# Optimization experiments

Measured on AMD Instinct MI355X. Metric: run time of the kernel, lower is better.

The kernel has to match this reference:

```python
import jax, jax.numpy as jnp
from jax import lax
import numpy as np

EPS = 1e-10


def setup_inputs() -> dict:
    key = jax.random.key(0)
    B, C, F, T = 32, 2, 257, 2000
    x = jax.random.uniform(key, (B, C, F, T), dtype=jnp.float32)  # magnitude-like, positive
    return {"input": x, "sample_length": 192}


def reference(input, sample_length):
    # Faithful jax version of BaseModel.forgetting_norm.
    # input: [B, C, F, T]
    B, C, F, T = input.shape
    x = input.reshape(B, C * F, T)
    dt = x.dtype
    # per-frame mean over channel*freq: [B, T]
    frame_mean = jnp.mean(x, axis=1)
    alpha = jnp.asarray((sample_length - 1) / (sample_length + 1), dtype=dt)
    idx = jnp.arange(T, dtype=dt)
    # torch code: alp = min((i-1)/(i+1), alpha); for i >= sample_length this equals alpha
    alp = jnp.minimum((idx - 1.0) / (idx + 1.0), alpha)  # [T]

    def step(mu, inp):
        a, m = inp  # scalars broadcast over batch: a [], m [B]
        mu = a * mu + (1.0 - a) * m
        return mu, mu

    mu0 = jnp.zeros((B,), dtype=dt)
    _, mus = lax.scan(step, mu0, (alp, frame_mean.T))  # mus: [T, B]
    mu = mus.T  # [B, T]
    out = x / (mu[:, None, :] + EPS)
    return out.reshape(B, C, F, T)
```

## Files before the change

### kernel.cpp

```cpp
#include <hip/hip_runtime.h>

#define EPS 1e-10f

constexpr int B  = 32;
constexpr int CF = 514;
constexpr int T  = 2000;
constexpr int T4 = T / 4;

__global__ __launch_bounds__(512) void k_frame_mean(const float* __restrict__ x,
                                                    float* __restrict__ fm) {
    __shared__ float lds[8][64];
    const int t  = blockIdx.x * 64 + threadIdx.x;
    const int b  = blockIdx.y;
    const int ty = threadIdx.y;

    float s = 0.0f;
    if (t < T) {
        const float* p = x + ((size_t)b * CF + ty) * T + t;
        #pragma unroll 4
        for (int cf = ty; cf < CF; cf += 8) {
            s += *p;
            p += 8 * (size_t)T;
        }
    }
    lds[ty][threadIdx.x] = s;
    __syncthreads();
    if (ty == 0 && t < T) {
        float tot = lds[0][threadIdx.x];
        #pragma unroll
        for (int k = 1; k < 8; ++k) tot += lds[k][threadIdx.x];
        fm[(size_t)b * T + t] = tot / (float)CF;
    }
}

__global__ __launch_bounds__(256) void k_scan_par(const float* __restrict__ fm,
                                                  const int* __restrict__ d_sl,
                                                  float* __restrict__ mu_out) {
    const int wave = threadIdx.x >> 6;
    const int lane = threadIdx.x & 63;
    const int b    = blockIdx.x * 4 + wave;
    if (b >= B) return;

    const int sl = d_sl[0];
    const float alpha = (float)((double)(sl - 1) / (double)(sl + 1));

    const float* __restrict__ m = fm + (size_t)b * T;
    float* __restrict__ o = mu_out + (size_t)b * T;

    const int t0 = lane * 32;

    float v[32];
    if (t0 + 32 <= T) {
        #pragma unroll
        for (int j = 0; j < 8; ++j)
            *(float4*)(v + 4 * j) = *(const float4*)(m + t0 + 4 * j);
    } else {
        #pragma unroll
        for (int j = 0; j < 32; ++j)
            v[j] = (t0 + j < T) ? m[t0 + j] : 0.0f;
    }

    float A = 1.0f, Bv = 0.0f;
    #pragma unroll
    for (int i = 0; i < 32; ++i) {
        const int t = t0 + i;
        const float ft = (float)t;
        const float a  = (t < T) ? fminf((ft - 1.0f) / (ft + 1.0f), alpha) : 1.0f;
        const float vv = (t < T) ? v[i] : 0.0f;
        Bv = a * Bv + (1.0f - a) * vv;
        A  = a * A;
    }

    float pA = A, pB = Bv;
    #pragma unroll
    for (int d = 1; d < 64; d <<= 1) {
        const float uA = __shfl_up(pA, d);
        const float uB = __shfl_up(pB, d);
        if (lane >= d) {
            pB = pA * uB + pB;
            pA = pA * uA;
        }
    }

    const float eB = __shfl_up(pB, 1);
    float mu = (lane == 0) ? 0.0f : eB;

    #pragma unroll
    for (int i = 0; i < 32; ++i) {
        const int t = t0 + i;
        if (t < T) {
            const float ft = (float)t;
            const float a  = fminf((ft - 1.0f) / (ft + 1.0f), alpha);
            mu = a * mu + (1.0f - a) * v[i];
            o[t] = mu;
        }
    }
}

__global__ __launch_bounds__(256) void k_norm(const float4* __restrict__ x,
                                              const float* __restrict__ mu,
                                              float4* __restrict__ out) {
    const int t4  = blockIdx.x * 256 + threadIdx.x;
    if (t4 >= T4) return;
    const int row = blockIdx.y;
    const int b   = row / CF;

    const size_t idx = (size_t)row * T4 + t4;
    const float4 v  = x[idx];
    const float4 m4 = *(const float4*)(mu + (size_t)b * T + (size_t)t4 * 4);

    float4 r;
    r.x = v.x / (m4.x + EPS);
    r.y = v.y / (m4.y + EPS);
    r.z = v.z / (m4.z + EPS);
    r.w = v.w / (m4.w + EPS);
    out[idx] = r;
}

extern "C" void kernel_launch(void* const* d_in, const int* in_sizes, int n_in,
                              void* d_out, int out_size, void* d_ws, size_t ws_size,
                              hipStream_t stream) {
    const float* x    = (const float*)d_in[0];
    const int*   d_sl = (const int*)d_in[1];
    float*       out  = (float*)d_out;

    float* fm = (float*)d_ws;
    float* mu = fm + (size_t)B * T;

    {
        dim3 grid((T + 63) / 64, B);
        dim3 block(64, 8);
        k_frame_mean<<<grid, block, 0, stream>>>(x, fm);
    }
    {
        k_scan_par<<<8, 256, 0, stream>>>(fm, d_sl, mu);
    }
    {
        dim3 grid((T4 + 255) / 256, B * CF);
        dim3 block(256);
        k_norm<<<grid, block, 0, stream>>>((const float4*)x, mu, (float4*)out);
    }
}
```

Measured before the change: 258.4 us.

## Fuse scan into normalization kernel with per-block redundant scan

```diff
diff --git a/kernel.cpp b/kernel.cpp
--- a/kernel.cpp
+++ b/kernel.cpp
@@ -5,7 +5,6 @@
 constexpr int B  = 32;
 constexpr int CF = 514;
 constexpr int T  = 2000;
-constexpr int T4 = T / 4;
 
 __global__ __launch_bounds__(512) void k_frame_mean(const float* __restrict__ x,
                                                     float* __restrict__ fm) {
@@ -33,88 +32,85 @@
     }
 }
 
-__global__ __launch_bounds__(256) void k_scan_par(const float* __restrict__ fm,
-                                                  const int* __restrict__ d_sl,
-                                                  float* __restrict__ mu_out) {
-    const int wave = threadIdx.x >> 6;
-    const int lane = threadIdx.x & 63;
-    const int b    = blockIdx.x * 4 + wave;
-    if (b >= B) return;
+__global__ __launch_bounds__(256) void k_scan_norm(const float* __restrict__ x,
+                                                   const float* __restrict__ fm,
+                                                   const int* __restrict__ d_sl,
+                                                   float* __restrict__ out) {
+    __shared__ float mu_win[64];
+    const int tx  = threadIdx.x & 63;
+    const int ty  = threadIdx.x >> 6;
+    const int bid = blockIdx.x;
+    const int b   = bid >> 5;
+    const int t0  = (bid & 31) * 64;
 
-    const int sl = d_sl[0];
-    const float alpha = (float)((double)(sl - 1) / (double)(sl + 1));
+    if (ty == 0) {
+        const int lane = tx;
+        const int sl   = d_sl[0];
+        const float alpha = (float)((double)(sl - 1) / (double)(sl + 1));
+        const float* __restrict__ m = fm + (size_t)b * T;
+        const int ts = lane * 32;
 
-    const float* __restrict__ m = fm + (size_t)b * T;
-    float* __restrict__ o = mu_out + (size_t)b * T;
+        float v[32];
+        if (ts + 32 <= T) {
+            #pragma unroll
+            for (int j = 0; j < 8; ++j)
+                *(float4*)(v + 4 * j) = *(const float4*)(m + ts + 4 * j);
+        } else {
+            #pragma unroll
+            for (int j = 0; j < 32; ++j)
+                v[j] = (ts + j < T) ? m[ts + j] : 0.0f;
+        }
 
-    const int t0 = lane * 32;
+        float A = 1.0f, Bv = 0.0f;
+        #pragma unroll
+        for (int i = 0; i < 32; ++i) {
+            const int tt = ts + i;
+            const float ft = (float)tt;
+            const float a  = (tt < T) ? fminf((ft - 1.0f) / (ft + 1.0f), alpha) : 1.0f;
+            const float vv = (tt < T) ? v[i] : 0.0f;
+            Bv = a * Bv + (1.0f - a) * vv;
+            A  = a * A;
+        }
 
-    float v[32];
-    if (t0 + 32 <= T) {
+        float pA = A, pB = Bv;
         #pragma unroll
-        for (int j = 0; j < 8; ++j)
-            *(float4*)(v + 4 * j) = *(const float4*)(m + t0 + 4 * j);
-    } else {
+        for (int d = 1; d < 64; d <<= 1) {
+            const float uA = __shfl_up(pA, d);
+            const float uB = __shfl_up(pB, d);
+            if (lane >= d) {
+                pB = pA * uB + pB;
+                pA = pA * uA;
+            }
+        }
+
+        const float eB = __shfl_up(pB, 1);
+        float muv = (lane == 0) ? 0.0f : eB;
+
         #pragma unroll
-        for (int j = 0; j < 32; ++j)
-            v[j] = (t0 + j < T) ? m[t0 + j] : 0.0f;
-    }
-
-    float A = 1.0f, Bv = 0.0f;
-    #pragma unroll
-    for (int i = 0; i < 32; ++i) {
-        const int t = t0 + i;
-        const float ft = (float)t;
-        const float a  = (t < T) ? fminf((ft - 1.0f) / (ft + 1.0f), alpha) : 1.0f;
-        const float vv = (t < T) ? v[i] : 0.0f;
-        Bv = a * Bv + (1.0f - a) * vv;
-        A  = a * A;
-    }
-
-    float pA = A, pB = Bv;
-    #pragma unroll
-    for (int d = 1; d < 64; d <<= 1) {
-        const float uA = __shfl_up(pA, d);
-        const float uB = __shfl_up(pB, d);
-        if (lane >= d) {
-            pB = pA * uB + pB;
-            pA = pA * uA;
+        for (int i = 0; i < 32; ++i) {
+            const int tt = ts + i;
+            if (tt < T) {
+                const float ft = (float)tt;
+                const float a  = fminf((ft - 1.0f) / (ft + 1.0f), alpha);
+                muv = a * muv + (1.0f - a) * v[i];
+                if (tt >= t0 && tt < t0 + 64) mu_win[tt - t0] = muv;
+            }
         }
     }
+    __syncthreads();
 
-    const float eB = __shfl_up(pB, 1);
-    float mu = (lane == 0) ? 0.0f : eB;
-
-    #pragma unroll
-    for (int i = 0; i < 32; ++i) {
-        const int t = t0 + i;
-        if (t < T) {
-            const float ft = (float)t;
-            const float a  = fminf((ft - 1.0f) / (ft + 1.0f), alpha);
-            mu = a * mu + (1.0f - a) * v[i];
-            o[t] = mu;
+    const int t = t0 + tx;
+    if (t < T) {
+        const float d = mu_win[tx] + EPS;
+        const float* p = x + ((size_t)b * CF + ty) * T + t;
+        float* q = out + ((size_t)b * CF + ty) * T + t;
+        #pragma unroll 4
+        for (int cf = ty; cf < CF; cf += 4) {
+            *q = *p / d;
+            p += 4 * (size_t)T;
+            q += 4 * (size_t)T;
         }
     }
-}
-
-__global__ __launch_bounds__(256) void k_norm(const float4* __restrict__ x,
-                                              const float* __restrict__ mu,
-                                              float4* __restrict__ out) {
-    const int t4  = blockIdx.x * 256 + threadIdx.x;
-    if (t4 >= T4) return;
-    const int row = blockIdx.y;
-    const int b   = row / CF;
-
-    const size_t idx = (size_t)row * T4 + t4;
-    const float4 v  = x[idx];
-    const float4 m4 = *(const float4*)(mu + (size_t)b * T + (size_t)t4 * 4);
-
-    float4 r;
-    r.x = v.x / (m4.x + EPS);
-    r.y = v.y / (m4.y + EPS);
-    r.z = v.z / (m4.z + EPS);
-    r.w = v.w / (m4.w + EPS);
-    out[idx] = r;
 }
 
 extern "C" void kernel_launch(void* const* d_in, const int* in_sizes, int n_in,
@@ -125,7 +121,6 @@
     float*       out  = (float*)d_out;
 
     float* fm = (float*)d_ws;
-    float* mu = fm + (size_t)B * T;
 
     {
         dim3 grid((T + 63) / 64, B);
@@ -133,11 +128,6 @@
         k_frame_mean<<<grid, block, 0, stream>>>(x, fm);
     }
     {
-        k_scan_par<<<8, 256, 0, stream>>>(fm, d_sl, mu);
-    }
-    {
-        dim3 grid((T4 + 255) / 256, B * CF);
-        dim3 block(256);
-        k_norm<<<grid, block, 0, stream>>>((const float4*)x, mu, (float4*)out);
+        k_scan_norm<<<dim3(1024), dim3(256), 0, stream>>>(x, fm, d_sl, out);
     }
 }
```

After: 279.6 us. +8.2%, slower.
